# Performance work log

Measured on AMD Instinct MI355X. Metric: run time of the kernel, lower is better.

Reference implementation:

```python
import jax, jax.numpy as jnp
import numpy as np

TAU = 0.1          # contrastive_temperature
EPS = 0.05         # property_epsilon
L_LOCAL_G, L_GLOBAL, L_SC_G, L_LOCAL_SC, G_PROP = 1.0, 0.8, 1.0, 0.8, 0.5
B = 4096
D = 256
NUM_PROPS = 4
N_ATOMS = 131072
N_MOTIFS = 32768


def setup_inputs() -> dict:
    key = jax.random.key(0)
    ks = jax.random.split(key, 10)
    return {
        "emb_g_mole": jax.random.normal(ks[0], (B, D), jnp.float32),
        "emb_g_frag": jax.random.normal(ks[1], (N_ATOMS, D), jnp.float32),
        "emb_sc_mole": jax.random.normal(ks[2], (B, D), jnp.float32),
        "emb_sc_shape": jax.random.normal(ks[3], (N_MOTIFS, D), jnp.float32),
        "emb_motif": jax.random.normal(ks[4], (N_MOTIFS, D), jnp.float32),
        "emb_shape": jax.random.normal(ks[5], (N_MOTIFS, D), jnp.float32),
        # scaled so duplicate rows are the only pairs within EPS (realistic sparse mask)
        "prop_pred": jax.random.normal(ks[6], (B, NUM_PROPS), jnp.float32) * 0.05,
        "prop_target": jax.random.normal(ks[7], (B, NUM_PROPS), jnp.float32) * 0.05,
        "batch_g": jax.random.randint(ks[8], (N_ATOMS,), 0, B, jnp.int32),
        "batch_sc": jax.random.randint(ks[9], (N_MOTIFS,), 0, B, jnp.int32),
    }


def _contrastive(emb, props):
    # SupervisedContrastiveLoss: normalized cosine logits, mask from sqrt(cdist) < eps
    n = emb.shape[0]
    e = emb / jnp.maximum(jnp.linalg.norm(emb, axis=1, keepdims=True), 1e-12)
    logits = jnp.matmul(e, e.T) / TAU                       # [n, n]
    log_probs = jax.nn.log_softmax(logits, axis=1)
    sq = jnp.sum(props * props, axis=1)
    d2 = jnp.maximum(sq[:, None] + sq[None, :] - 2.0 * jnp.matmul(props, props.T), 0.0)
    dd = jnp.sqrt(jnp.sqrt(d2)) + 1e-8                      # cdist(...).sqrt() + 1e-8
    mask = (dd < EPS) & (~jnp.eye(n, dtype=bool))           # fill_diagonal_(0)
    cnt = jnp.sum(mask, axis=1)
    row_loss = -jnp.sum(jnp.where(mask, log_probs, 0.0), axis=1) / jnp.maximum(cnt, 1)
    valid = cnt > 0
    nvalid = jnp.sum(valid)
    loss = jnp.sum(jnp.where(valid, row_loss, 0.0)) / jnp.maximum(nvalid, 1)
    return jnp.where(nvalid > 0, loss, 0.0)


def _frag_alignment(emb_g_frag, emb_motif, batch_g, batch_sc):
    ones_g = jnp.ones((emb_g_frag.shape[0],), emb_g_frag.dtype)
    ones_s = jnp.ones((emb_motif.shape[0],), emb_motif.dtype)
    cnt_g = jax.ops.segment_sum(ones_g, batch_g, num_segments=B)
    cnt_s = jax.ops.segment_sum(ones_s, batch_sc, num_segments=B)
    mean_g = jax.ops.segment_sum(emb_g_frag, batch_g, num_segments=B) / jnp.maximum(cnt_g, 1.0)[:, None]
    mean_s = jax.ops.segment_sum(emb_motif, batch_sc, num_segments=B) / jnp.maximum(cnt_s, 1.0)[:, None]
    norms = jnp.linalg.norm(mean_g - mean_s, axis=1)
    valid = (cnt_g > 0) & (cnt_s > 0)
    batch_size = batch_g.max().astype(emb_g_frag.dtype) + 1.0
    return jnp.sum(jnp.where(valid, norms, 0.0)) / batch_size


def reference(emb_g_mole, emb_g_frag, emb_sc_mole, emb_sc_shape, emb_motif,
              emb_shape, prop_pred, prop_target, batch_g, batch_sc):
    l_local_g = _frag_alignment(emb_g_frag, emb_motif, batch_g, batch_sc)
    combined_emb = jnp.concatenate([emb_g_mole, emb_sc_mole], axis=0)    # [2B, d]
    combined_props = jnp.concatenate([prop_pred, prop_pred], axis=0)      # [2B, p]
    l_contr = _contrastive(combined_emb, combined_props)
    l_global = l_contr          # same inputs in both calls -> identical value
    l_local_sc = l_contr
    l_sc_g = jnp.mean(jnp.linalg.norm(emb_sc_shape - emb_shape, axis=1))  # AlignmentLoss mean
    l_prop = jnp.mean((prop_pred - prop_target) ** 2)                     # MSELoss
    l_hes = (L_LOCAL_G * l_local_g + L_GLOBAL * l_global + L_SC_G * l_sc_g
             + L_LOCAL_SC * l_local_sc + G_PROP * l_prop)
    # stacked: [l_hes, l_local_g, l_global, l_sc_g, l_local_sc, l_prop]
    return jnp.stack([l_hes, l_local_g, l_global, l_sc_g, l_local_sc, l_prop])
```

## Files before the change

kernel.cpp:

```cpp
#include <hip/hip_runtime.h>
#include <hip/hip_bf16.h>
#include <stdint.h>

typedef unsigned short u16;
typedef float f32x4 __attribute__((ext_vector_type(4)));
typedef short s16x8 __attribute__((ext_vector_type(8)));
typedef u16   u16x8 __attribute__((ext_vector_type(8)));
typedef u16   u16x4 __attribute__((ext_vector_type(4)));
typedef uint32_t u32x4 __attribute__((ext_vector_type(4)));

#define B_      4096
#define D_      256
#define NA_     131072
#define NM_     32768
#define N2_     8192
#define THR4    6.2499950e-6f
#define K2E     14.426950408889634f
#define LN2_    0.6931471805599453f
#define CAPG    96
#define CAPS    40

#define NS_   1024
#define NG_   2080
#define NT_   256
#define NTOT_ 3360
#define NR_   2336

#define OFF_CNT_G   0u
#define OFF_CNT_S   16384u
#define OFF_NB      32768u
#define OFF_SCAL    49152u
#define OFF_S       65536u
#define ZERO_BYTES  98304u
#define OFF_T       98304u
#define OFF_C       131072u
#define OFF_PLIST   163840u
#define OFF_LIST_G  688128u
#define OFF_LIST_S  2260992u
#define OFF_E       2916352u
#define WS_NEED     7110656u

__device__ inline float wave_sum(float v) {
#pragma unroll
  for (int m = 1; m < 64; m <<= 1) v += __shfl_xor(v, m, 64);
  return v;
}
__device__ inline int wave_sum_i(int v) {
#pragma unroll
  for (int m = 1; m < 64; m <<= 1) v += __shfl_xor(v, m, 64);
  return v;
}
__device__ inline u16 f2bf(float f) {
  uint32_t u = __float_as_uint(f);
  uint32_t r = (u + 0x7FFFu + ((u >> 16) & 1u)) >> 16;
  return (u16)r;
}
__device__ inline float bf2f(u16 v) { return __uint_as_float(((uint32_t)v) << 16); }

__device__ inline f32x4 ldnt4(const float* p) {
  return __builtin_nontemporal_load((const f32x4*)(p));
}

__device__ inline void gload16(const u16* __restrict__ g, u16* l) {
  __builtin_amdgcn_global_load_lds(
      (const __attribute__((address_space(1))) uint32_t*)g,
      (__attribute__((address_space(3))) uint32_t*)l, 16, 0, 0);
}

__global__ void k_zero(u32x4* __restrict__ p) {
  u32x4 z = {0u, 0u, 0u, 0u};
  p[blockIdx.x * 256 + threadIdx.x] = z;
}

__global__ __launch_bounds__(256) void k_fuseA(
    const int* __restrict__ bg, const int* __restrict__ bs,
    int* __restrict__ cntg, int* __restrict__ cnts, int* __restrict__ bmax,
    int* __restrict__ listg, int* __restrict__ lists,
    const float* __restrict__ gm, const float* __restrict__ scm,
    const float* __restrict__ scs, const float* __restrict__ shp,
    const float* __restrict__ pp,
    u16* __restrict__ E, int* __restrict__ nb, int* __restrict__ plist,
    float* __restrict__ scal) {
  int t = threadIdx.x, w = t >> 6, lane = t & 63;
  int blk = blockIdx.x;

  if (blk % 17 == 0) {
    int aid = blk / 17;
    int i = aid * 256 + t;
    int b = -1;
    if (i < NA_) {
      b = bg[i];
      int pos = atomicAdd(&cntg[b], 1);
      if (pos < CAPG) listg[b * CAPG + pos] = i;
    }
    if (i < NM_) {
      int b2 = bs[i];
      int pos = atomicAdd(&cnts[b2], 1);
      if (pos < CAPS) lists[b2 * CAPS + pos] = i;
    }
    int m = b;
#pragma unroll
    for (int k = 1; k < 64; k <<= 1) m = max(m, __shfl_xor(m, k, 64));
    if ((t & 63) == 0 && m >= 0) atomicMax(bmax, m);
    return;
  }
  int r1 = blk - blk / 17 - 1;

  if (!(r1 & 1)) {
    int a = r1 >> 1;
    f32x4 pa = *(const f32x4*)(pp + (size_t)a * 4);
    for (int b = t; b < B_; b += 256) {
      f32x4 pb = *(const f32x4*)(pp + (size_t)b * 4);
      float dx = pa.x - pb.x, dy = pa.y - pb.y, dz = pa.z - pb.z, dw = pa.w - pb.w;
      float d2 = dx * dx + dy * dy + dz * dz + dw * dw;
      if (d2 < THR4) {
        int pos = atomicAdd(&nb[a], 1);
        if (pos < 32) plist[a * 32 + pos] = b;
      }
    }
    return;
  }
  int r3 = r1 >> 1;

  if (!(r3 & 1)) {
    int r = (r3 >> 1) * 4 + w;
    const float* src = (r < B_) ? gm + (size_t)r * D_ : scm + (size_t)(r - B_) * D_;
    f32x4 v = ldnt4(src + lane * 4);
    float ss = v.x * v.x + v.y * v.y + v.z * v.z + v.w * v.w;
    ss = wave_sum(ss);
    float inv = 1.f / fmaxf(sqrtf(ss), 1e-12f);
    u16x4 o;
    o.x = f2bf(v.x * inv); o.y = f2bf(v.y * inv);
    o.z = f2bf(v.z * inv); o.w = f2bf(v.w * inv);
    *(u16x4*)(E + (size_t)r * D_ + lane * 4) = o;
  } else {
    int wg = (r3 >> 1) * 4 + w;
    float acc = 0.f;
    for (int r = wg; r < NM_; r += 8192) {
      f32x4 va = ldnt4(scs + (size_t)r * D_ + lane * 4);
      f32x4 vb = ldnt4(shp + (size_t)r * D_ + lane * 4);
      float dx = va.x - vb.x, dy = va.y - vb.y, dz = va.z - vb.z, dw = va.w - vb.w;
      float ss = wave_sum(dx * dx + dy * dy + dz * dz + dw * dw);
      if (lane == 0) acc += sqrtf(ss);
    }
    __shared__ float sr4[4];
    if (lane == 0) sr4[w] = acc;
    __syncthreads();
    if (t == 0) atomicAdd(&scal[1], sr4[0] + sr4[1] + sr4[2] + sr4[3]);
  }
}

__device__ inline void wave_row_sum(const float* __restrict__ src,
                                    const int* __restrict__ list,
                                    int off, int cnt, int lane, f32x4* accs) {
  f32x4 a0 = {0.f,0.f,0.f,0.f}, a1 = a0, a2 = a0, a3 = a0;
  f32x4 a4 = a0, a5 = a0, a6 = a0, a7 = a0;
  for (int base = 0; base < cnt; base += 64) {
    int n = min(cnt - base, 64);
    int idx = (lane < n) ? list[off + base + lane] : 0;
    int k = 0;
    for (; k + 7 < n; k += 8) {
      int i0 = __shfl(idx, k,     64), i1 = __shfl(idx, k + 1, 64);
      int i2 = __shfl(idx, k + 2, 64), i3 = __shfl(idx, k + 3, 64);
      int i4 = __shfl(idx, k + 4, 64), i5 = __shfl(idx, k + 5, 64);
      int i6 = __shfl(idx, k + 6, 64), i7 = __shfl(idx, k + 7, 64);
      a0 += ldnt4(src + (size_t)i0 * D_ + lane * 4);
      a1 += ldnt4(src + (size_t)i1 * D_ + lane * 4);
      a2 += ldnt4(src + (size_t)i2 * D_ + lane * 4);
      a3 += ldnt4(src + (size_t)i3 * D_ + lane * 4);
      a4 += ldnt4(src + (size_t)i4 * D_ + lane * 4);
      a5 += ldnt4(src + (size_t)i5 * D_ + lane * 4);
      a6 += ldnt4(src + (size_t)i6 * D_ + lane * 4);
      a7 += ldnt4(src + (size_t)i7 * D_ + lane * 4);
    }
    for (; k < n; k++) {
      int i0 = __shfl(idx, k, 64);
      a0 += ldnt4(src + (size_t)i0 * D_ + lane * 4);
    }
  }
  *accs = ((a0 + a1) + (a2 + a3)) + ((a4 + a5) + (a6 + a7));
}

__global__ __launch_bounds__(256) void k_fuseB(
    const u16* __restrict__ E,
    const float* __restrict__ fg, const float* __restrict__ fm,
    const int* __restrict__ cntg, const int* __restrict__ cnts,
    const int* __restrict__ listg, const int* __restrict__ lists,
    const int* __restrict__ nb, const int* __restrict__ plist,
    float* __restrict__ S, float* __restrict__ T, int* __restrict__ C,
    float* __restrict__ scal) {
  __shared__ __align__(16) u16 As[128 * 32];
  __shared__ __align__(16) u16 Bs[128 * 32];
  int blk = blockIdx.x;
  int tid = threadIdx.x, lane = tid & 63, wid = tid >> 6;

  int64_t p = (int64_t)blk * NS_;
  int srem = (int)(p % NTOT_);
  if (srem < NS_) {
    int sid = (int)(p / NTOT_);
    int b = sid * 4 + wid;
    int cg = cntg[b], cs = cnts[b];
    f32x4 sg, ss;
    wave_row_sum(fg, listg, b * CAPG, min(cg, CAPG), lane, &sg);
    wave_row_sum(fm, lists, b * CAPS, min(cs, CAPS), lane, &ss);
    float ig = 1.f / fmaxf((float)cg, 1.f);
    float is = 1.f / fmaxf((float)cs, 1.f);
    float dx = sg.x * ig - ss.x * is, dy = sg.y * ig - ss.y * is;
    float dz = sg.z * ig - ss.z * is, dw = sg.w * ig - ss.w * is;
    float v = wave_sum(dx * dx + dy * dy + dz * dz + dw * dw);
    __shared__ float r2[4];
    if (lane == 0) r2[wid] = (cg > 0 && cs > 0) ? sqrtf(v) : 0.f;
    __syncthreads();
    if (tid == 0) {
      float s = r2[0] + r2[1] + r2[2] + r2[3];
      if (s != 0.f) atomicAdd(&scal[0], s);
    }
    return;
  }

  int r = blk - (int)((p + NTOT_ - 1) / NTOT_);
  int64_t q = (int64_t)r * NG_;
  int grem = (int)(q % NR_);

  if (grem >= NG_) {
    int tix = r - (int)((q + NR_ - 1) / NR_);
#pragma unroll
    for (int k8 = 0; k8 < 8; k8++) {
      int i = tix * 32 + wid * 8 + k8;
      int a = i & (B_ - 1);
      int n = min(nb[a], 32);
      u16x4 vi = *(const u16x4*)(E + (size_t)i * D_ + lane * 4);
      float ex = bf2f(vi.x), ey = bf2f(vi.y), ez = bf2f(vi.z), ew = bf2f(vi.w);
      float acc = -(ex * ex + ey * ey + ez * ez + ew * ew);
      for (int k = 0; k < n; k++) {
        int b = plist[a * 32 + k];
        u16x4 v1 = *(const u16x4*)(E + (size_t)b * D_ + lane * 4);
        u16x4 v2 = *(const u16x4*)(E + (size_t)(b + B_) * D_ + lane * 4);
        acc += ex * bf2f(v1.x) + ey * bf2f(v1.y) + ez * bf2f(v1.z) + ew * bf2f(v1.w);
        acc += ex * bf2f(v2.x) + ey * bf2f(v2.y) + ez * bf2f(v2.z) + ew * bf2f(v2.w);
      }
      acc = wave_sum(acc);
      if (lane == 0) { T[i] = 10.0f * acc; C[i] = 2 * n - 1; }
    }
    return;
  }

  int t = (int)(q / NR_);
  int bi = (int)((129.0f - sqrtf(129.0f * 129.0f - 8.0f * (float)t)) * 0.5f);
  while ((bi + 1) * (129 - (bi + 1)) / 2 <= t) bi++;
  while (bi * (129 - bi) / 2 > t) bi--;
  int bj = bi + (t - bi * (129 - bi) / 2);

  int row0 = bi * 128, col0 = bj * 128;
  int wr = wid >> 1, wc = wid & 1;

  int rsub = lane >> 2;
  int csw  = (((lane & 3) ^ (rsub & 3)) << 3);

  f32x4 acc[4][4];
#pragma unroll
  for (int mi = 0; mi < 4; mi++)
#pragma unroll
    for (int ni = 0; ni < 4; ni++) {
      f32x4 z = {0.f, 0.f, 0.f, 0.f};
      acc[mi][ni] = z;
    }

  for (int kc = 0; kc < 8; ++kc) {
    __syncthreads();
#pragma unroll
    for (int it = 0; it < 2; it++) {
      int s = wid * 2 + it;
      int rr = s * 16 + rsub;
      gload16(E + (size_t)(row0 + rr) * D_ + kc * 32 + csw, As + s * 512);
      gload16(E + (size_t)(col0 + rr) * D_ + kc * 32 + csw, Bs + s * 512);
    }
    __syncthreads();
    s16x8 af[4], bfr[4];
#pragma unroll
    for (int mi = 0; mi < 4; mi++) {
      int rA = wr * 64 + mi * 16 + (lane & 15);
      int addr = rA * 64 + (((lane >> 4) * 16) ^ ((rA & 3) << 4));
      af[mi] = *(const s16x8*)((const char*)As + addr);
    }
#pragma unroll
    for (int ni = 0; ni < 4; ni++) {
      int rB = wc * 64 + ni * 16 + (lane & 15);
      int addr = rB * 64 + (((lane >> 4) * 16) ^ ((rB & 3) << 4));
      bfr[ni] = *(const s16x8*)((const char*)Bs + addr);
    }
#pragma unroll
    for (int mi = 0; mi < 4; mi++)
#pragma unroll
      for (int ni = 0; ni < 4; ni++)
        acc[mi][ni] = __builtin_amdgcn_mfma_f32_16x16x32_bf16(af[mi], bfr[ni], acc[mi][ni], 0, 0, 0);
  }

  int g = lane >> 4, cl = lane & 15;
  float colsum[4] = {0.f, 0.f, 0.f, 0.f};
#pragma unroll
  for (int mi = 0; mi < 4; mi++) {
#pragma unroll
    for (int reg = 0; reg < 4; ++reg) {
      int gi = row0 + wr * 64 + mi * 16 + g * 4 + reg;
      float vs = 0.f;
#pragma unroll
      for (int ni = 0; ni < 4; ni++) {
        float e = exp2f(acc[mi][ni][reg] * K2E - K2E);
        vs += e;
        colsum[ni] += e;
      }
#pragma unroll
      for (int m = 1; m < 16; m <<= 1) vs += __shfl_xor(vs, m, 64);
      if (cl == 0) atomicAdd(&S[gi], vs);
    }
  }
  if (bi != bj) {
#pragma unroll
    for (int ni = 0; ni < 4; ni++) {
      float cs = colsum[ni];
      cs += __shfl_xor(cs, 16, 64);
      cs += __shfl_xor(cs, 32, 64);
      if (g == 0) atomicAdd(&S[col0 + wc * 64 + ni * 16 + cl], cs);
    }
  }
}

__global__ void k_final(const float* __restrict__ S, const float* __restrict__ T,
                        const int* __restrict__ C, const float* __restrict__ scal,
                        const float* __restrict__ pp, const float* __restrict__ pt,
                        float* __restrict__ out) {
  float sp = 0.f;
  for (int i = threadIdx.x; i < B_ * 4; i += 256) {
    float d = pp[i] - pt[i];
    sp += d * d;
  }
  float rls = 0.f; int nv = 0;
  for (int i = threadIdx.x; i < N2_; i += 256) {
    int ci = C[i];
    if (ci > 0) { rls += (10.0f + __log2f(S[i]) * LN2_) - T[i] / (float)ci; nv++; }
  }
  rls = wave_sum(rls);
  sp  = wave_sum(sp);
  nv  = wave_sum_i(nv);
  __shared__ float r1[4], r3[4]; __shared__ int r2[4];
  int lane = threadIdx.x & 63, w = threadIdx.x >> 6;
  if (lane == 0) { r1[w] = rls; r2[w] = nv; r3[w] = sp; }
  __syncthreads();
  if (threadIdx.x == 0) {
    float rtot = r1[0] + r1[1] + r1[2] + r1[3];
    int nvt = r2[0] + r2[1] + r2[2] + r2[3];
    float sptot = r3[0] + r3[1] + r3[2] + r3[3];
    float l_contr = nvt > 0 ? rtot / (float)nvt : 0.f;
    int bmax = ((const int*)scal)[3];
    float bs = (float)bmax + 1.0f;
    float l_local_g = scal[0] / bs;
    float l_sc = scal[1] / (float)NM_;
    float l_prop = sptot / (float)(B_ * 4);
    float l_hes = 1.0f * l_local_g + 0.8f * l_contr + 1.0f * l_sc + 0.8f * l_contr + 0.5f * l_prop;
    out[0] = l_hes; out[1] = l_local_g; out[2] = l_contr;
    out[3] = l_sc;  out[4] = l_contr;   out[5] = l_prop;
  }
}

extern "C" void kernel_launch(void* const* d_in, const int* in_sizes, int n_in,
                              void* d_out, int out_size, void* d_ws, size_t ws_size,
                              hipStream_t stream) {
  if (ws_size < WS_NEED) return;
  const float* gm  = (const float*)d_in[0];
  const float* fg  = (const float*)d_in[1];
  const float* scm = (const float*)d_in[2];
  const float* scs = (const float*)d_in[3];
  const float* mot = (const float*)d_in[4];
  const float* shp = (const float*)d_in[5];
  const float* pp  = (const float*)d_in[6];
  const float* pt  = (const float*)d_in[7];
  const int* bg = (const int*)d_in[8];
  const int* bs = (const int*)d_in[9];
  float* out = (float*)d_out;
  char* ws = (char*)d_ws;

  int* cntg  = (int*)(ws + OFF_CNT_G);
  int* cnts  = (int*)(ws + OFF_CNT_S);
  int* nb    = (int*)(ws + OFF_NB);
  float* scal = (float*)(ws + OFF_SCAL);
  float* S   = (float*)(ws + OFF_S);
  float* T   = (float*)(ws + OFF_T);
  int* C     = (int*)(ws + OFF_C);
  int* plist = (int*)(ws + OFF_PLIST);
  int* listg = (int*)(ws + OFF_LIST_G);
  int* lists = (int*)(ws + OFF_LIST_S);
  u16* E     = (u16*)(ws + OFF_E);

  k_zero<<<24, 256, 0, stream>>>((u32x4*)ws);
  k_fuseA<<<8704, 256, 0, stream>>>(bg, bs, cntg, cnts, (int*)scal + 3,
                                    listg, lists, gm, scm, scs, shp, pp,
                                    E, nb, plist, scal);
  k_fuseB<<<NTOT_, 256, 0, stream>>>(E, fg, mot, cntg, cnts, listg, lists,
                                     nb, plist, S, T, C, scal);
  k_final<<<1, 256, 0, stream>>>(S, T, C, scal, pp, pt, out);
}
```

Measured before the change: 200.1 us.

## Pre-convert fragment embeddings to bf16 and batch property-neighbor rows per block

When the workspace is large enough, k_fuseA gains stages that convert the full fragment and motif embedding tables to bf16 copies. k_fuseB then gathers these half-width rows, with each half-wave loading 8 bf16 values per row, to build the per-molecule fragment means. Separately, the property-neighbour search now handles 16 anchor rows per block instead of one, which cuts that stage from 4096 blocks to 256 and reuses each loaded property row 16 times. The bf16 path adds a full read of both fp32 tables plus a write of the bf16 copies before the gather, and the rounding can shift the alignment loss slightly.

```diff
diff --git a/kernel.cpp b/kernel.cpp
--- a/kernel.cpp
+++ b/kernel.cpp
@@ -38,7 +38,10 @@
 #define OFF_LIST_G  688128u
 #define OFF_LIST_S  2260992u
 #define OFF_E       2916352u
-#define WS_NEED     7110656u
+#define WS_SMALL    7110656u
+#define OFF_FGB     7110656u
+#define OFF_FMB     74219520u
+#define WS_BIG      90996736u
 
 __device__ inline float wave_sum(float v) {
 #pragma unroll
@@ -59,6 +62,9 @@
 
 __device__ inline f32x4 ldnt4(const float* p) {
   return __builtin_nontemporal_load((const f32x4*)(p));
+}
+__device__ inline u16x8 ldnt8(const u16* p) {
+  return __builtin_nontemporal_load((const u16x8*)(p));
 }
 
 __device__ inline void gload16(const u16* __restrict__ g, u16* l) {
@@ -79,74 +85,144 @@
     const float* __restrict__ gm, const float* __restrict__ scm,
     const float* __restrict__ scs, const float* __restrict__ shp,
     const float* __restrict__ pp,
+    const float* __restrict__ fg, const float* __restrict__ fm,
+    u16* __restrict__ fgb, u16* __restrict__ fmb,
     u16* __restrict__ E, int* __restrict__ nb, int* __restrict__ plist,
-    float* __restrict__ scal) {
+    float* __restrict__ scal, int big) {
   int t = threadIdx.x, w = t >> 6, lane = t & 63;
   int blk = blockIdx.x;
-
-  if (blk % 17 == 0) {
-    int aid = blk / 17;
-    int i = aid * 256 + t;
-    int b = -1;
-    if (i < NA_) {
-      b = bg[i];
-      int pos = atomicAdd(&cntg[b], 1);
-      if (pos < CAPG) listg[b * CAPG + pos] = i;
-    }
-    if (i < NM_) {
-      int b2 = bs[i];
-      int pos = atomicAdd(&cnts[b2], 1);
-      if (pos < CAPS) lists[b2 * CAPS + pos] = i;
-    }
-    int m = b;
-#pragma unroll
-    for (int k = 1; k < 64; k <<= 1) m = max(m, __shfl_xor(m, k, 64));
-    if ((t & 63) == 0 && m >= 0) atomicMax(bmax, m);
-    return;
-  }
-  int r1 = blk - blk / 17 - 1;
-
-  if (!(r1 & 1)) {
-    int a = r1 >> 1;
-    f32x4 pa = *(const f32x4*)(pp + (size_t)a * 4);
-    for (int b = t; b < B_; b += 256) {
-      f32x4 pb = *(const f32x4*)(pp + (size_t)b * 4);
-      float dx = pa.x - pb.x, dy = pa.y - pb.y, dz = pa.z - pb.z, dw = pa.w - pb.w;
-      float d2 = dx * dx + dy * dy + dz * dz + dw * dw;
-      if (d2 < THR4) {
-        int pos = atomicAdd(&nb[a], 1);
-        if (pos < 32) plist[a * 32 + pos] = b;
-      }
-    }
-    return;
-  }
-  int r3 = r1 >> 1;
-
-  if (!(r3 & 1)) {
-    int r = (r3 >> 1) * 4 + w;
-    const float* src = (r < B_) ? gm + (size_t)r * D_ : scm + (size_t)(r - B_) * D_;
-    f32x4 v = ldnt4(src + lane * 4);
-    float ss = v.x * v.x + v.y * v.y + v.z * v.z + v.w * v.w;
-    ss = wave_sum(ss);
-    float inv = 1.f / fmaxf(sqrtf(ss), 1e-12f);
-    u16x4 o;
-    o.x = f2bf(v.x * inv); o.y = f2bf(v.y * inv);
-    o.z = f2bf(v.z * inv); o.w = f2bf(v.w * inv);
-    *(u16x4*)(E + (size_t)r * D_ + lane * 4) = o;
-  } else {
-    int wg = (r3 >> 1) * 4 + w;
-    float acc = 0.f;
-    for (int r = wg; r < NM_; r += 8192) {
-      f32x4 va = ldnt4(scs + (size_t)r * D_ + lane * 4);
-      f32x4 vb = ldnt4(shp + (size_t)r * D_ + lane * 4);
-      float dx = va.x - vb.x, dy = va.y - vb.y, dz = va.z - vb.z, dw = va.w - vb.w;
-      float ss = wave_sum(dx * dx + dy * dy + dz * dz + dw * dw);
-      if (lane == 0) acc += sqrtf(ss);
-    }
-    __shared__ float sr4[4];
-    if (lane == 0) sr4[w] = acc;
-    __syncthreads();
-    if (t == 0) atomicAdd(&scal[1], sr4[0] + sr4[1] + sr4[2] + sr4[3]);
+  int ntot = big ? 7424 : 4864;
+
+  {
+    int64_t p = (int64_t)blk * 512;
+    int rem = (int)(p % ntot);
+    if (rem < 512) {
+      int aid = (int)(p / ntot);
+      int i = aid * 256 + t;
+      int b = -1;
+      if (i < NA_) {
+        b = bg[i];
+        int pos = atomicAdd(&cntg[b], 1);
+        if (pos < CAPG) listg[b * CAPG + pos] = i;
+      }
+      if (i < NM_) {
+        int b2 = bs[i];
+        int pos = atomicAdd(&cnts[b2], 1);
+        if (pos < CAPS) lists[b2 * CAPS + pos] = i;
+      }
+      int m = b;
+#pragma unroll
+      for (int k = 1; k < 64; k <<= 1) m = max(m, __shfl_xor(m, k, 64));
+      if ((t & 63) == 0 && m >= 0) atomicMax(bmax, m);
+      return;
+    }
+    blk -= (int)((p + ntot - 1) / ntot);
+    ntot -= 512;
+  }
+
+  {
+    int64_t p = (int64_t)blk * 256;
+    int rem = (int)(p % ntot);
+    if (rem < 256) {
+      int pid = (int)(p / ntot);
+      int a0 = pid * 16;
+      __shared__ f32x4 pa_s[16];
+      if (t < 16) pa_s[t] = *(const f32x4*)(pp + (size_t)(a0 + t) * 4);
+      __syncthreads();
+      for (int it = 0; it < 16; ++it) {
+        int b = it * 256 + t;
+        f32x4 pb = *(const f32x4*)(pp + (size_t)b * 4);
+#pragma unroll
+        for (int j = 0; j < 16; ++j) {
+          f32x4 pa = pa_s[j];
+          float dx = pa.x - pb.x, dy = pa.y - pb.y, dz = pa.z - pb.z, dw = pa.w - pb.w;
+          float d2 = dx * dx + dy * dy + dz * dz + dw * dw;
+          if (d2 < THR4) {
+            int a = a0 + j;
+            int pos = atomicAdd(&nb[a], 1);
+            if (pos < 32) plist[a * 32 + pos] = b;
+          }
+        }
+      }
+      return;
+    }
+    blk -= (int)((p + ntot - 1) / ntot);
+    ntot -= 256;
+  }
+
+  {
+    int64_t p = (int64_t)blk * 2048;
+    int rem = (int)(p % ntot);
+    if (rem < 2048) {
+      int nid = (int)(p / ntot);
+      int r = nid * 4 + w;
+      const float* src = (r < B_) ? gm + (size_t)r * D_ : scm + (size_t)(r - B_) * D_;
+      f32x4 v = ldnt4(src + lane * 4);
+      float ss = v.x * v.x + v.y * v.y + v.z * v.z + v.w * v.w;
+      ss = wave_sum(ss);
+      float inv = 1.f / fmaxf(sqrtf(ss), 1e-12f);
+      u16x4 o;
+      o.x = f2bf(v.x * inv); o.y = f2bf(v.y * inv);
+      o.z = f2bf(v.z * inv); o.w = f2bf(v.w * inv);
+      *(u16x4*)(E + (size_t)r * D_ + lane * 4) = o;
+      return;
+    }
+    blk -= (int)((p + ntot - 1) / ntot);
+    ntot -= 2048;
+  }
+
+  {
+    int64_t p = (int64_t)blk * 2048;
+    int rem = (int)(p % ntot);
+    if (rem < 2048) {
+      int lid = (int)(p / ntot);
+      int wg = lid * 4 + w;
+      float acc = 0.f;
+      for (int r = wg; r < NM_; r += 8192) {
+        f32x4 va = ldnt4(scs + (size_t)r * D_ + lane * 4);
+        f32x4 vb = ldnt4(shp + (size_t)r * D_ + lane * 4);
+        float dx = va.x - vb.x, dy = va.y - vb.y, dz = va.z - vb.z, dw = va.w - vb.w;
+        float ss = wave_sum(dx * dx + dy * dy + dz * dz + dw * dw);
+        if (lane == 0) acc += sqrtf(ss);
+      }
+      __shared__ float sr4[4];
+      if (lane == 0) sr4[w] = acc;
+      __syncthreads();
+      if (t == 0) atomicAdd(&scal[1], sr4[0] + sr4[1] + sr4[2] + sr4[3]);
+      return;
+    }
+    blk -= (int)((p + ntot - 1) / ntot);
+    ntot -= 2048;
+  }
+
+  {
+    int64_t p = (int64_t)blk * 2048;
+    int rem = (int)(p % ntot);
+    if (rem < 2048) {
+      int cid = (int)(p / ntot);
+#pragma unroll 4
+      for (int rr = 0; rr < 16; ++rr) {
+        int row = cid * 64 + w * 16 + rr;
+        f32x4 v = ldnt4(fg + (size_t)row * D_ + lane * 4);
+        u16x4 o;
+        o.x = f2bf(v.x); o.y = f2bf(v.y); o.z = f2bf(v.z); o.w = f2bf(v.w);
+        *(u16x4*)(fgb + (size_t)row * D_ + lane * 4) = o;
+      }
+      return;
+    }
+    blk -= (int)((p + ntot - 1) / ntot);
+    ntot -= 2048;
+  }
+
+  {
+#pragma unroll 4
+    for (int rr = 0; rr < 16; ++rr) {
+      int row = blk * 64 + w * 16 + rr;
+      f32x4 v = ldnt4(fm + (size_t)row * D_ + lane * 4);
+      u16x4 o;
+      o.x = f2bf(v.x); o.y = f2bf(v.y); o.z = f2bf(v.z); o.w = f2bf(v.w);
+      *(u16x4*)(fmb + (size_t)row * D_ + lane * 4) = o;
+    }
   }
 }
 
@@ -181,14 +257,68 @@
   *accs = ((a0 + a1) + (a2 + a3)) + ((a4 + a5) + (a6 + a7));
 }
 
+#define BF8ADD(vv, okk, LL, HH)                                              \
+  if (okk) {                                                                 \
+    LL.x += bf2f(vv[0]); LL.y += bf2f(vv[1]); LL.z += bf2f(vv[2]); LL.w += bf2f(vv[3]); \
+    HH.x += bf2f(vv[4]); HH.y += bf2f(vv[5]); HH.z += bf2f(vv[6]); HH.w += bf2f(vv[7]); \
+  }
+
+__device__ inline void wave_row_sum_b16(const u16* __restrict__ src,
+                                        const int* __restrict__ list,
+                                        int off, int cnt, int lane,
+                                        f32x4* lo, f32x4* hi) {
+  f32x4 z = {0.f, 0.f, 0.f, 0.f};
+  f32x4 l0 = z, l1 = z, l2 = z, l3 = z, h0 = z, h1 = z, h2 = z, h3 = z;
+  int half = lane >> 5;
+  int dl = lane & 31;
+  for (int base = 0; base < cnt; base += 64) {
+    int n = min(cnt - base, 64);
+    int idx = (lane < n) ? list[off + base + lane] : 0;
+    int npair = (n + 1) >> 1;
+    int j = 0;
+    for (; j + 7 < npair; j += 8) {
+      int e0 = 2 * j + half;
+      int i0 = __shfl(idx, e0,      64), i1 = __shfl(idx, e0 + 2,  64);
+      int i2 = __shfl(idx, e0 + 4,  64), i3 = __shfl(idx, e0 + 6,  64);
+      int i4 = __shfl(idx, e0 + 8,  64), i5 = __shfl(idx, e0 + 10, 64);
+      int i6 = __shfl(idx, e0 + 12, 64), i7 = __shfl(idx, e0 + 14, 64);
+      u16x8 v0 = ldnt8(src + (size_t)i0 * D_ + dl * 8);
+      u16x8 v1 = ldnt8(src + (size_t)i1 * D_ + dl * 8);
+      u16x8 v2 = ldnt8(src + (size_t)i2 * D_ + dl * 8);
+      u16x8 v3 = ldnt8(src + (size_t)i3 * D_ + dl * 8);
+      u16x8 v4 = ldnt8(src + (size_t)i4 * D_ + dl * 8);
+      u16x8 v5 = ldnt8(src + (size_t)i5 * D_ + dl * 8);
+      u16x8 v6 = ldnt8(src + (size_t)i6 * D_ + dl * 8);
+      u16x8 v7 = ldnt8(src + (size_t)i7 * D_ + dl * 8);
+      BF8ADD(v0, e0      < n, l0, h0); BF8ADD(v1, e0 + 2  < n, l1, h1);
+      BF8ADD(v2, e0 + 4  < n, l2, h2); BF8ADD(v3, e0 + 6  < n, l3, h3);
+      BF8ADD(v4, e0 + 8  < n, l0, h0); BF8ADD(v5, e0 + 10 < n, l1, h1);
+      BF8ADD(v6, e0 + 12 < n, l2, h2); BF8ADD(v7, e0 + 14 < n, l3, h3);
+    }
+    for (; j < npair; j++) {
+      int e = 2 * j + half;
+      int i0 = __shfl(idx, e, 64);
+      u16x8 v = ldnt8(src + (size_t)i0 * D_ + dl * 8);
+      BF8ADD(v, e < n, l0, h0);
+    }
+  }
+  f32x4 L = (l0 + l1) + (l2 + l3), H = (h0 + h1) + (h2 + h3);
+  L.x += __shfl_xor(L.x, 32, 64); L.y += __shfl_xor(L.y, 32, 64);
+  L.z += __shfl_xor(L.z, 32, 64); L.w += __shfl_xor(L.w, 32, 64);
+  H.x += __shfl_xor(H.x, 32, 64); H.y += __shfl_xor(H.y, 32, 64);
+  H.z += __shfl_xor(H.z, 32, 64); H.w += __shfl_xor(H.w, 32, 64);
+  *lo = L; *hi = H;
+}
+
 __global__ __launch_bounds__(256) void k_fuseB(
     const u16* __restrict__ E,
     const float* __restrict__ fg, const float* __restrict__ fm,
+    const u16* __restrict__ fgb, const u16* __restrict__ fmb,
     const int* __restrict__ cntg, const int* __restrict__ cnts,
     const int* __restrict__ listg, const int* __restrict__ lists,
     const int* __restrict__ nb, const int* __restrict__ plist,
     float* __restrict__ S, float* __restrict__ T, int* __restrict__ C,
-    float* __restrict__ scal) {
+    float* __restrict__ scal, int big) {
   __shared__ __align__(16) u16 As[128 * 32];
   __shared__ __align__(16) u16 Bs[128 * 32];
   int blk = blockIdx.x;
@@ -200,16 +330,30 @@
     int sid = (int)(p / NTOT_);
     int b = sid * 4 + wid;
     int cg = cntg[b], cs = cnts[b];
-    f32x4 sg, ss;
-    wave_row_sum(fg, listg, b * CAPG, min(cg, CAPG), lane, &sg);
-    wave_row_sum(fm, lists, b * CAPS, min(cs, CAPS), lane, &ss);
-    float ig = 1.f / fmaxf((float)cg, 1.f);
-    float is = 1.f / fmaxf((float)cs, 1.f);
-    float dx = sg.x * ig - ss.x * is, dy = sg.y * ig - ss.y * is;
-    float dz = sg.z * ig - ss.z * is, dw = sg.w * ig - ss.w * is;
-    float v = wave_sum(dx * dx + dy * dy + dz * dz + dw * dw);
+    float loc;
+    if (big) {
+      f32x4 gl, gh, sl, sh;
+      wave_row_sum_b16(fgb, listg, b * CAPG, min(cg, CAPG), lane, &gl, &gh);
+      wave_row_sum_b16(fmb, lists, b * CAPS, min(cs, CAPS), lane, &sl, &sh);
+      float ig = 1.f / fmaxf((float)cg, 1.f);
+      float is = 1.f / fmaxf((float)cs, 1.f);
+      f32x4 d0 = gl * ig - sl * is;
+      f32x4 d1 = gh * ig - sh * is;
+      loc = d0.x * d0.x + d0.y * d0.y + d0.z * d0.z + d0.w * d0.w
+          + d1.x * d1.x + d1.y * d1.y + d1.z * d1.z + d1.w * d1.w;
+      loc = wave_sum(loc) * 0.5f;
+    } else {
+      f32x4 sg, ss;
+      wave_row_sum(fg, listg, b * CAPG, min(cg, CAPG), lane, &sg);
+      wave_row_sum(fm, lists, b * CAPS, min(cs, CAPS), lane, &ss);
+      float ig = 1.f / fmaxf((float)cg, 1.f);
+      float is = 1.f / fmaxf((float)cs, 1.f);
+      float dx = sg.x * ig - ss.x * is, dy = sg.y * ig - ss.y * is;
+      float dz = sg.z * ig - ss.z * is, dw = sg.w * ig - ss.w * is;
+      loc = wave_sum(dx * dx + dy * dy + dz * dz + dw * dw);
+    }
     __shared__ float r2[4];
-    if (lane == 0) r2[wid] = (cg > 0 && cs > 0) ? sqrtf(v) : 0.f;
+    if (lane == 0) r2[wid] = (cg > 0 && cs > 0) ? sqrtf(loc) : 0.f;
     __syncthreads();
     if (tid == 0) {
       float s = r2[0] + r2[1] + r2[2] + r2[3];
@@ -366,7 +510,9 @@
 extern "C" void kernel_launch(void* const* d_in, const int* in_sizes, int n_in,
                               void* d_out, int out_size, void* d_ws, size_t ws_size,
                               hipStream_t stream) {
-  if (ws_size < WS_NEED) return;
+  if (ws_size < WS_SMALL) return;
+  int big = (ws_size >= WS_BIG) ? 1 : 0;
+
   const float* gm  = (const float*)d_in[0];
   const float* fg  = (const float*)d_in[1];
   const float* scm = (const float*)d_in[2];
@@ -391,12 +537,14 @@
   int* listg = (int*)(ws + OFF_LIST_G);
   int* lists = (int*)(ws + OFF_LIST_S);
   u16* E     = (u16*)(ws + OFF_E);
+  u16* fgb   = (u16*)(ws + OFF_FGB);
+  u16* fmb   = (u16*)(ws + OFF_FMB);
 
   k_zero<<<24, 256, 0, stream>>>((u32x4*)ws);
-  k_fuseA<<<8704, 256, 0, stream>>>(bg, bs, cntg, cnts, (int*)scal + 3,
-                                    listg, lists, gm, scm, scs, shp, pp,
-                                    E, nb, plist, scal);
-  k_fuseB<<<NTOT_, 256, 0, stream>>>(E, fg, mot, cntg, cnts, listg, lists,
-                                     nb, plist, S, T, C, scal);
+  k_fuseA<<<big ? 7424 : 4864, 256, 0, stream>>>(
+      bg, bs, cntg, cnts, (int*)scal + 3, listg, lists,
+      gm, scm, scs, shp, pp, fg, mot, fgb, fmb, E, nb, plist, scal, big);
+  k_fuseB<<<NTOT_, 256, 0, stream>>>(E, fg, mot, fgb, fmb, cntg, cnts,
+                                     listg, lists, nb, plist, S, T, C, scal, big);
   k_final<<<1, 256, 0, stream>>>(S, T, C, scal, pp, pt, out);
 }
```

New measurement: 218.8 us. +9.4%, slower.
